# Kernel optimization log

Measured on AMD Instinct MI355X. Metric: run time of the kernel, lower is better.

## Reference

```python
import jax, jax.numpy as jnp
import numpy as np


def conv2d(x, w, b):
    pad = (w.shape[-1] - 1) // 2
    y = jax.lax.conv_general_dilated(x, w, (1, 1), [(pad, pad), (pad, pad)],
                                     dimension_numbers=('NCHW', 'OIHW', 'NCHW'))
    return y + b[None, :, None, None]


def mish(x):
    return x * jnp.tanh(jax.nn.softplus(x))


def setup_inputs() -> dict:
    key = jax.random.key(0)
    ks = jax.random.split(key, 8)
    B, C, H, W = 8, 16, 256, 256
    s = 0.1
    return dict(
        x=jax.random.normal(ks[0], (B, C, H, W), jnp.float32),
        W1=jax.random.normal(ks[1], (4, 1, 3, 3), jnp.float32) * s,      # conv1: 1->4, k=3
        b1=jnp.zeros((4,), jnp.float32),
        Wred=jax.random.normal(ks[2], (1, 4, 1, 1), jnp.float32) * s,    # involution reduce 4->1
        bred=jnp.zeros((1,), jnp.float32),
        Wspan=jax.random.normal(ks[3], (9, 1, 1, 1), jnp.float32) * s,   # involution span 1->k^2
        bspan=jnp.zeros((9,), jnp.float32),
        W2=jax.random.normal(ks[4], (C, 4 * C, 3, 3), jnp.float32) * s,  # conv2: 4C->C, k=3
        b2=jnp.zeros((C,), jnp.float32),
        Weca=jax.random.normal(ks[5], (3,), jnp.float32) * s,            # ECA 1D conv kernel
    )


def reference(x, W1, b1, Wred, bred, Wspan, bspan, W2, b2, Weca):
    B, C, H, W = x.shape
    H2 = H // 2
    K2 = 9  # 3x3 involution kernel
    # per-channel 1->4 conv + Mish: vectorize the Python channel loop by folding C into batch
    xs = x.reshape(B * C, 1, H, W)
    f = mish(conv2d(xs, W1, b1))                      # (B*C, 4, H, W)
    top, bot = f[:, :, :H2], f[:, :, H2:]             # each (B*C, 4, H2, W)
    # involution2(y1, y2): dynamic per-pixel 3x3 kernel from bottom half, applied to top half
    ker = conv2d(jax.nn.relu(conv2d(bot, Wred, bred)), Wspan, bspan)   # (B*C, 9, H2, W)
    patches = jax.lax.conv_general_dilated_patches(
        top, (3, 3), (1, 1), [(1, 1), (1, 1)],
        dimension_numbers=('NCHW', 'OIHW', 'NCHW'))                    # (B*C, 4*9, H2, W), channel-major
    patches = patches.reshape(B * C, 4, K2, H2, W)
    top_inv = (patches * ker[:, None]).sum(axis=2)                     # (B*C, 4, H2, W)
    # shuffle/concat: out channel-block i = [inv_top_i ; bottom_{(i+1) % C}] along height
    ti = top_inv.reshape(B, C, 4, H2, W)
    bo = bot.reshape(B, C, 4, H2, W)
    shuffled = jnp.concatenate([ti, jnp.roll(bo, -1, axis=1)], axis=3)  # (B, C, 4, H, W)
    shuffled = shuffled.reshape(B, 4 * C, H, W)
    out = mish(conv2d(shuffled, W2, b2))               # (B, C, H, W)
    # ECA: gate from global-avg-pooled `out`, 1D cross-correlation (k=3, pad=1) over channels
    pooled = out.mean(axis=(2, 3))                     # (B, C)
    yp = jnp.pad(pooled, ((0, 0), (1, 1)))
    gate = jax.nn.sigmoid(Weca[0] * yp[:, :-2] + Weca[1] * yp[:, 1:-1] + Weca[2] * yp[:, 2:])
    return x * gate[:, :, None, None]
```

## Files before the change

### kernel.cpp

```cpp
#include <hip/hip_runtime.h>
#include <hip/hip_bf16.h>

#define H 256
#define Wd 256
#define H2 128

typedef unsigned short ushort_t;
typedef __attribute__((ext_vector_type(8))) short short8;
typedef __attribute__((ext_vector_type(4))) float f32x4;

__device__ __forceinline__ float mishf(float v){
  if (v > 15.f) return v;
  float e = __expf(v);
  float w = e*(e+2.f);
  return v * w * __builtin_amdgcn_rcpf(w + 2.f);
}
__device__ __forceinline__ float mish_s(float v){
  float e = __expf(v);
  float w = e*(e+2.f);
  return v * w * __builtin_amdgcn_rcpf(w + 2.f);
}

__device__ __forceinline__ ushort_t f2bf(float f){
  unsigned int u = __float_as_uint(f);
  u += 0x7fffu + ((u >> 16) & 1u);
  return (ushort_t)(u >> 16);
}
__device__ __forceinline__ unsigned packbf(float a, float b){
  return (unsigned)f2bf(a) | ((unsigned)f2bf(b) << 16);
}
__device__ __forceinline__ float lo16(unsigned u){
  return __uint_as_float(u << 16);
}
__device__ __forceinline__ float hi16(unsigned u){
  return __uint_as_float(u & 0xffff0000u);
}


__global__ void k0_pack(const float* __restrict__ W2, ushort_t* __restrict__ wpack)
{
  int idx = blockIdx.x*128 + threadIdx.x;
  if (idx >= 1152) return;
  int lane  = idx & 63;
  int s     = (idx >> 6) % 9;
  int khalf = idx / 576;
  int n = lane & 15, g = lane >> 4;
  unsigned int w[4];
#pragma unroll
  for (int h = 0; h < 4; ++h){
    int ch0 = khalf*32 + g*8 + 2*h;
    unsigned lo = f2bf(W2[(n*64 + ch0  )*9 + s]);
    unsigned hi = f2bf(W2[(n*64 + ch0+1)*9 + s]);
    w[h] = lo | (hi << 16);
  }
  *(uint4*)(wpack + (size_t)idx*8) = make_uint4(w[0], w[1], w[2], w[3]);
}

#define FT_STRIDE 560
__global__ __launch_bounds__(256) void k12h(
    const float* __restrict__ x, const float* __restrict__ W1,
    const float* __restrict__ b1, const float* __restrict__ Wred,
    const float* __restrict__ bred, const float* __restrict__ Wspan,
    const float* __restrict__ bspan, ushort_t* __restrict__ shuf)
{
  __shared__ __align__(16) char ftl[18*FT_STRIDE];

  int bid = blockIdx.x;
  int n   = bid >> 5;
  int t   = bid & 31;
  int itop0 = (t >> 2) * 16;
  int j0    = (t & 3) * 64;
  int tid = threadIdx.x;
  const float* xp = x + (size_t)n * (H*Wd);
  const float4 f4z = make_float4(0.f,0.f,0.f,0.f);

  float w1r[36], b1r[4], wsp[9], bsp[9], wredr[4];
  float bredr = bred[0];
#pragma unroll
  for (int k=0;k<36;k++) w1r[k] = W1[k];
#pragma unroll
  for (int m=0;m<4;m++){ b1r[m] = b1[m]; wredr[m] = Wred[m]; }
#pragma unroll
  for (int k=0;k<9;k++){ wsp[k] = Wspan[k]; bsp[k] = bspan[k]; }

#pragma unroll
  for (int pi0 = 0; pi0 < 2; ++pi0){
    int pi = tid + pi0*256;
    if (pi < 306){
      int r  = pi / 17;
      int q  = pi - r*17;
      int frow  = itop0 - 1 + r;
      int fcol0 = j0 - 2 + 4*q;
      uint4 o0 = make_uint4(0u,0u,0u,0u), o1 = make_uint4(0u,0u,0u,0u);
      if ((unsigned)frow < 128u){
        float v[3][8];
        int cA = fcol0 - 2, cB = fcol0 + 2;
#pragma unroll
        for (int rr=0; rr<3; ++rr){
          int xr = frow - 1 + rr;
          bool rok = (xr >= 0);
          const float* rp = xp + (size_t)xr*Wd;
          float4 a = (rok && cA >= 0)   ? *(const float4*)(rp + cA) : f4z;
          float4 b = (rok && cB <= 252) ? *(const float4*)(rp + cB) : f4z;
          v[rr][0]=a.x; v[rr][1]=a.y; v[rr][2]=a.z; v[rr][3]=a.w;
          v[rr][4]=b.x; v[rr][5]=b.y; v[rr][6]=b.z; v[rr][7]=b.w;
        }
        float s[4][4];
#pragma unroll
        for (int m=0;m<4;m++)
#pragma unroll
          for (int p=0;p<4;p++) s[m][p] = b1r[m];
#pragma unroll
        for (int ky=0;ky<3;ky++)
#pragma unroll
          for (int kx=0;kx<3;kx++){
#pragma unroll
            for (int m=0;m<4;m++){
              float wv = w1r[m*9+ky*3+kx];
#pragma unroll
              for (int p=0;p<4;p++)
                s[m][p] = fmaf(v[ky][p+1+kx], wv, s[m][p]);
            }
          }
        unsigned pw[8];
#pragma unroll
        for (int p=0;p<4;p++){
          bool ok = (unsigned)(fcol0+p) < 256u;
          pw[p*2]   = ok ? packbf(mish_s(s[0][p]), mish_s(s[1][p])) : 0u;
          pw[p*2+1] = ok ? packbf(mish_s(s[2][p]), mish_s(s[3][p])) : 0u;
        }
        o0 = make_uint4(pw[0],pw[1],pw[2],pw[3]);
        o1 = make_uint4(pw[4],pw[5],pw[6],pw[7]);
      }
      char* dst = ftl + r*FT_STRIDE + q*32;
      *(uint4*)dst = o0;
      *(uint4*)(dst+16) = o1;
    }
  }

  int lr  = tid >> 4;
  int lc4 = (tid & 15) * 4;
  int trow = itop0 + lr;
  int bq = n >> 4, cq = n & 15;
  int jc = j0 + lc4;

  float vb[3][6];
  bool look = (jc >= 4);
  bool hiok = (jc <= 248);
#pragma unroll
  for (int rr=0; rr<3; ++rr){
    int xr = 127 + trow + rr;
    bool rok = (xr < 256);
    const float* rp = xp + (size_t)xr*Wd + jc;
    float4 m = rok ? *(const float4*)rp : f4z;
    float lw = (rok && look) ? rp[-1] : 0.f;
    float rw = (rok && hiok) ? rp[4]  : 0.f;
    vb[rr][0]=lw; vb[rr][1]=m.x; vb[rr][2]=m.y; vb[rr][3]=m.z; vb[rr][4]=m.w; vb[rr][5]=rw;
  }
  float fb[4][4];
#pragma unroll
  for (int m=0;m<4;m++)
#pragma unroll
    for (int p=0;p<4;p++){
      float s = b1r[m];
#pragma unroll
      for (int ky=0;ky<3;ky++)
#pragma unroll
        for (int kx=0;kx<3;kx++)
          s = fmaf(vb[ky][p+kx], w1r[m*9+ky*3+kx], s);
      fb[m][p] = mish_s(s);
    }
  int cdst = (cq + 15) & 15;
  size_t bbase = ((size_t)(bq*16 + cdst))*65536 + (size_t)(128+trow)*256 + jc;
  {
    unsigned w0 = packbf(fb[0][0], fb[1][0]), w1 = packbf(fb[2][0], fb[3][0]);
    unsigned w2 = packbf(fb[0][1], fb[1][1]), w3 = packbf(fb[2][1], fb[3][1]);
    *(uint4*)(shuf + bbase*4) = make_uint4(w0,w1,w2,w3);
    unsigned w4 = packbf(fb[0][2], fb[1][2]), w5 = packbf(fb[2][2], fb[3][2]);
    unsigned w6 = packbf(fb[0][3], fb[1][3]), w7 = packbf(fb[2][3], fb[3][3]);
    *(uint4*)(shuf + (bbase+2)*4) = make_uint4(w4,w5,w6,w7);
  }
  float gv[4];
#pragma unroll
  for (int p=0;p<4;p++){
    float s = bredr;
#pragma unroll
    for (int m=0;m<4;m++) s = fmaf(fb[m][p], wredr[m], s);
    gv[p] = fmaxf(s, 0.f);
  }

  __syncthreads();

  float Aa[4][4], Bb[4][4];
#pragma unroll
  for (int m=0;m<4;m++)
#pragma unroll
    for (int p=0;p<4;p++){ Aa[m][p]=0.f; Bb[m][p]=0.f; }

#pragma unroll
  for (int ky=0;ky<3;ky++){
    const char* src = ftl + (lr+ky)*FT_STRIDE + lc4*8;
    float f0[8], f1[8], f2[8], f3[8];
#pragma unroll
    for (int jj=0;jj<4;jj++){
      uint4 u = *(const uint4*)(src + jj*16);
      f0[2*jj]   = lo16(u.x); f1[2*jj]   = hi16(u.x);
      f2[2*jj]   = lo16(u.y); f3[2*jj]   = hi16(u.y);
      f0[2*jj+1] = lo16(u.z); f1[2*jj+1] = hi16(u.z);
      f2[2*jj+1] = lo16(u.w); f3[2*jj+1] = hi16(u.w);
    }
#pragma unroll
    for (int kx=0;kx<3;kx++){
      float ws = wsp[ky*3+kx], bs = bsp[ky*3+kx];
#pragma unroll
      for (int p=0;p<4;p++){
        int ix = p + 1 + kx;
        Aa[0][p] = fmaf(f0[ix], ws, Aa[0][p]); Bb[0][p] = fmaf(f0[ix], bs, Bb[0][p]);
        Aa[1][p] = fmaf(f1[ix], ws, Aa[1][p]); Bb[1][p] = fmaf(f1[ix], bs, Bb[1][p]);
        Aa[2][p] = fmaf(f2[ix], ws, Aa[2][p]); Bb[2][p] = fmaf(f2[ix], bs, Bb[2][p]);
        Aa[3][p] = fmaf(f3[ix], ws, Aa[3][p]); Bb[3][p] = fmaf(f3[ix], bs, Bb[3][p]);
      }
    }
  }

  float o[4][4];
#pragma unroll
  for (int m=0;m<4;m++)
#pragma unroll
    for (int p=0;p<4;p++)
      o[m][p] = fmaf(gv[p], Aa[m][p], Bb[m][p]);

  size_t pbase = ((size_t)(bq*16 + cq))*65536 + (size_t)trow*256 + jc;
  {
    unsigned w0 = packbf(o[0][0], o[1][0]), w1 = packbf(o[2][0], o[3][0]);
    unsigned w2 = packbf(o[0][1], o[1][1]), w3 = packbf(o[2][1], o[3][1]);
    *(uint4*)(shuf + pbase*4) = make_uint4(w0,w1,w2,w3);
    unsigned w4 = packbf(o[0][2], o[1][2]), w5 = packbf(o[2][2], o[3][2]);
    unsigned w6 = packbf(o[0][3], o[1][3]), w7 = packbf(o[2][3], o[3][3]);
    *(uint4*)(shuf + (pbase+2)*4) = make_uint4(w4,w5,w6,w7);
  }
}

__global__ __launch_bounds__(256) void k3_conv2(
    const ushort_t* __restrict__ shuf, const ushort_t* __restrict__ wpack,
    const float* __restrict__ b2, float* __restrict__ scratch)
{
  __shared__ f32x4 mg[2][8][64];
  __shared__ float pacc[16];

  int bid0 = blockIdx.x;
  int bid  = (bid0 & 7)*256 + (bid0 >> 3);
  int b   = bid >> 8;
  int t   = bid & 255;
  int rb  = t >> 3;
  int cb  = t & 7;
  int tid = threadIdx.x;
  int lane = tid & 63;
  int n = lane & 15;
  int g = lane >> 4;
  int wid = tid >> 6;
  int colhalf = wid & 1;
  int khalf   = wid >> 1;

  if (tid < 16) pacc[tid] = 0.f;

  const short8* wp = (const short8*)wpack + (size_t)khalf*576 + lane;
  short8 afr[9];
#pragma unroll
  for (int s = 0; s < 9; ++s) afr[s] = wp[s*64];

  f32x4 acc[8];
#pragma unroll
  for (int r = 0; r < 8; ++r) acc[r] = f32x4{0.f,0.f,0.f,0.f};

  int r0 = rb*8 - 1;
  int c  = cb*32 - 1 + colhalf*16 + n;
  int p0 = khalf*8 + g*2;
  const ushort_t* sp = shuf + ((size_t)(b*16 + p0))*262144;

#pragma unroll
  for (int hr = 0; hr < 10; ++hr){
    int grow = r0 + hr;
    bool rok = (unsigned)grow < 256u;
    uint2 va[3], vb[3];
#pragma unroll
    for (int kx = 0; kx < 3; ++kx){
      int gcol = c + kx;
      uint2 a = make_uint2(0u,0u), bv = make_uint2(0u,0u);
      if (rok && (unsigned)gcol < 256u){
        const ushort_t* pp = sp + (size_t)(grow*256 + gcol)*4;
        a  = *(const uint2*)pp;
        bv = *(const uint2*)(pp + 262144);
      }
      va[kx] = a; vb[kx] = bv;
    }
#pragma unroll
    for (int kx = 0; kx < 3; ++kx){
      union { uint4 u; short8 s; } cv;
      cv.u = make_uint4(va[kx].x, va[kx].y, vb[kx].x, vb[kx].y);
#pragma unroll
      for (int ky = 0; ky < 3; ++ky){
        int orow = hr - ky;
        if (orow >= 0 && orow < 8){
          acc[orow] = __builtin_amdgcn_mfma_f32_16x16x32_bf16(
              afr[ky*3+kx], cv.s, acc[orow], 0, 0, 0);
        }
      }
    }
  }

  if (khalf == 1){
#pragma unroll
    for (int r = 0; r < 8; ++r) mg[colhalf][r][lane] = acc[r];
  }
  __syncthreads();

  if (khalf == 0){
    float b2v[4];
#pragma unroll
    for (int q = 0; q < 4; ++q) b2v[q] = b2[g*4 + q];
    float po[4] = {0.f, 0.f, 0.f, 0.f};
#pragma unroll
    for (int r = 0; r < 8; ++r){
      f32x4 o = acc[r] + mg[colhalf][r][lane];
#pragma unroll
      for (int q = 0; q < 4; ++q) po[q] += mishf(o[q] + b2v[q]);
    }
#pragma unroll
    for (int q = 0; q < 4; ++q){
#pragma unroll
      for (int mk = 1; mk < 16; mk <<= 1) po[q] += __shfl_xor(po[q], mk);
    }
    if (n == 0){
#pragma unroll
      for (int q = 0; q < 4; ++q) atomicAdd(&pacc[g*4 + q], po[q]);
    }
  }
  __syncthreads();
  if (tid < 16) scratch[bid*16 + tid] = pacc[tid];
}

__global__ void k4_gate(const float* __restrict__ scratch,
                        const float* __restrict__ Weca,
                        float* __restrict__ gate)
{
  __shared__ float rr[16][16];
  __shared__ float pool[16];
  int b = blockIdx.x;
  int t = threadIdx.x;
  int oc = t & 15, ch = t >> 4;
  float s = 0.f;
  for (int u = 0; u < 16; ++u)
    s += scratch[(size_t)(b*256 + ch*16 + u)*16 + oc];
  rr[ch][oc] = s;
  __syncthreads();
  if (t < 16){
    float tot = 0.f;
#pragma unroll
    for (int k = 0; k < 16; ++k) tot += rr[k][t];
    pool[t] = tot * (1.0f/65536.0f);
  }
  __syncthreads();
  if (t < 16){
    float pm = (t > 0)  ? pool[t-1] : 0.f;
    float p0 = pool[t];
    float pp = (t < 15) ? pool[t+1] : 0.f;
    float z = Weca[0]*pm + Weca[1]*p0 + Weca[2]*pp;
    gate[b*16 + t] = 1.f/(1.f + __expf(-z));
  }
}

__global__ __launch_bounds__(256) void k5_scale(
    const f32x4* __restrict__ x4, const float* __restrict__ gate,
    f32x4* __restrict__ out4)
{
  int idx = blockIdx.x*256 + threadIdx.x;
  float g = gate[idx >> 14];
  f32x4 v = x4[idx] * g;
  __builtin_nontemporal_store(v, &out4[idx]);
}

extern "C" void kernel_launch(void* const* d_in, const int* in_sizes, int n_in,
                              void* d_out, int out_size, void* d_ws, size_t ws_size,
                              hipStream_t stream)
{
  const float* x     = (const float*)d_in[0];
  const float* W1    = (const float*)d_in[1];
  const float* b1    = (const float*)d_in[2];
  const float* Wred  = (const float*)d_in[3];
  const float* bred  = (const float*)d_in[4];
  const float* Wspan = (const float*)d_in[5];
  const float* bspan = (const float*)d_in[6];
  const float* W2    = (const float*)d_in[7];
  const float* b2    = (const float*)d_in[8];
  const float* Weca  = (const float*)d_in[9];

  ushort_t* shuf    = (ushort_t*)d_ws;
  float*    gate    = (float*)((char*)d_ws + 67108864);
  ushort_t* wpack   = (ushort_t*)((char*)d_ws + 67108864 + 1024);
  float*    scratch = (float*)d_out;

  k0_pack<<<9, 128, 0, stream>>>(W2, wpack);
  k12h   <<<4096, 256, 0, stream>>>(x, W1, b1, Wred, bred, Wspan, bspan, shuf);
  k3_conv2<<<2048, 256, 0, stream>>>(shuf, wpack, b2, scratch);
  k4_gate<<<8, 256, 0, stream>>>(scratch, Weca, gate);
  k5_scale<<<8192, 256, 0, stream>>>((const f32x4*)x, gate, (f32x4*)d_out);
}
```

Before: 91.13 us.

## Replace LDS-tiled conv1/involution kernel with register-sliding per-thread column strips

The fused conv1+Mish+involution kernel drops its shared-memory tile and barrier. Each thread now owns a 4-row by 4-column strip and slides a 3-row register window down the rows, recomputing halo feature columns itself instead of sharing them through LDS. The grid shrinks from 4096 to 1024 blocks, with a block-index swizzle, so each thread does more work. The scale kernel also switches to a nontemporal load; the tradeoffs are redundant halo compute and higher register pressure.

```diff
diff --git a/kernel.cpp b/kernel.cpp
--- a/kernel.cpp
+++ b/kernel.cpp
@@ -56,22 +56,23 @@
   *(uint4*)(wpack + (size_t)idx*8) = make_uint4(w[0], w[1], w[2], w[3]);
 }
 
-#define FT_STRIDE 560
-__global__ __launch_bounds__(256) void k12h(
+__global__ __launch_bounds__(256) void k12c(
     const float* __restrict__ x, const float* __restrict__ W1,
     const float* __restrict__ b1, const float* __restrict__ Wred,
     const float* __restrict__ bred, const float* __restrict__ Wspan,
     const float* __restrict__ bspan, ushort_t* __restrict__ shuf)
 {
-  __shared__ __align__(16) char ftl[18*FT_STRIDE];
-
-  int bid = blockIdx.x;
-  int n   = bid >> 5;
-  int t   = bid & 31;
-  int itop0 = (t >> 2) * 16;
-  int j0    = (t & 3) * 64;
-  int tid = threadIdx.x;
-  const float* xp = x + (size_t)n * (H*Wd);
+  int bid0 = blockIdx.x;
+  int bid  = (bid0 & 7)*128 + (bid0 >> 3);
+  int n    = bid >> 3;
+  int L    = (bid & 7)*256 + threadIdx.x;
+  int band = L >> 6;
+  int strip= L & 63;
+  int r0 = band*4;
+  int jc = strip*4;
+  const float* xp = x + (size_t)n*65536;
+  bool jl = (jc == 0), jh = (jc == 252);
+  int bq = n >> 4, cq = n & 15;
   const float4 f4z = make_float4(0.f,0.f,0.f,0.f);
 
   float w1r[36], b1r[4], wsp[9], bsp[9], wredr[4];
@@ -83,162 +84,135 @@
 #pragma unroll
   for (int k=0;k<9;k++){ wsp[k] = Wspan[k]; bsp[k] = bspan[k]; }
 
-#pragma unroll
-  for (int pi0 = 0; pi0 < 2; ++pi0){
-    int pi = tid + pi0*256;
-    if (pi < 306){
-      int r  = pi / 17;
-      int q  = pi - r*17;
-      int frow  = itop0 - 1 + r;
-      int fcol0 = j0 - 2 + 4*q;
-      uint4 o0 = make_uint4(0u,0u,0u,0u), o1 = make_uint4(0u,0u,0u,0u);
-      if ((unsigned)frow < 128u){
-        float v[3][8];
-        int cA = fcol0 - 2, cB = fcol0 + 2;
-#pragma unroll
-        for (int rr=0; rr<3; ++rr){
-          int xr = frow - 1 + rr;
-          bool rok = (xr >= 0);
-          const float* rp = xp + (size_t)xr*Wd;
-          float4 a = (rok && cA >= 0)   ? *(const float4*)(rp + cA) : f4z;
-          float4 b = (rok && cB <= 252) ? *(const float4*)(rp + cB) : f4z;
-          v[rr][0]=a.x; v[rr][1]=a.y; v[rr][2]=a.z; v[rr][3]=a.w;
-          v[rr][4]=b.x; v[rr][5]=b.y; v[rr][6]=b.z; v[rr][7]=b.w;
+#define LOADB(row_, dst_) { \
+    int rw = (row_); \
+    bool rok = (rw < 256); \
+    const float* rp = xp + rw*256 + jc; \
+    float4 m_ = rok ? *(const float4*)rp : f4z; \
+    float l_ = (rok && !jl) ? rp[-1] : 0.f; \
+    float r_ = (rok && !jh) ? rp[4]  : 0.f; \
+    dst_[0]=l_; dst_[1]=m_.x; dst_[2]=m_.y; dst_[3]=m_.z; dst_[4]=m_.w; dst_[5]=r_; }
+
+#define LOADT(row_, dst_) { \
+    int rw = (row_); \
+    bool rok = (rw >= 0); \
+    const float* rp = xp + rw*256 + jc; \
+    float4 m_ = rok ? *(const float4*)rp : f4z; \
+    float4 l_ = (rok && !jl) ? *(const float4*)(rp-4) : f4z; \
+    float4 r_ = (rok && !jh) ? *(const float4*)(rp+4) : f4z; \
+    dst_[0]=l_.z; dst_[1]=l_.w; dst_[2]=m_.x; dst_[3]=m_.y; \
+    dst_[4]=m_.z; dst_[5]=m_.w; dst_[6]=r_.x; dst_[7]=r_.y; }
+
+  float gv[4][4];
+  {
+    float xb[3][6];
+    LOADB(127+r0, xb[0]);
+    LOADB(128+r0, xb[1]);
+    int cdst = (cq + 15) & 15;
+    size_t bplane = ((size_t)(bq*16 + cdst))*65536;
+#pragma unroll
+    for (int rr=0; rr<4; ++rr){
+      LOADB(129+r0+rr, xb[(rr+2)%3]);
+      float fbv[4][4];
+#pragma unroll
+      for (int m=0;m<4;m++)
+#pragma unroll
+        for (int p=0;p<4;p++){
+          float s = b1r[m];
+#pragma unroll
+          for (int ky=0;ky<3;ky++){
+            const float* xr = xb[(rr+ky)%3];
+#pragma unroll
+            for (int kx=0;kx<3;kx++)
+              s = fmaf(xr[p+kx], w1r[m*9+ky*3+kx], s);
+          }
+          fbv[m][p] = mish_s(s);
         }
-        float s[4][4];
-#pragma unroll
-        for (int m=0;m<4;m++)
-#pragma unroll
-          for (int p=0;p<4;p++) s[m][p] = b1r[m];
-#pragma unroll
-        for (int ky=0;ky<3;ky++)
+      size_t base = bplane + (size_t)(128+r0+rr)*256 + jc;
+      unsigned pw[8];
+#pragma unroll
+      for (int p=0;p<4;p++){
+        pw[p*2]   = packbf(fbv[0][p], fbv[1][p]);
+        pw[p*2+1] = packbf(fbv[2][p], fbv[3][p]);
+      }
+      *(uint4*)(shuf + base*4)     = make_uint4(pw[0],pw[1],pw[2],pw[3]);
+      *(uint4*)(shuf + (base+2)*4) = make_uint4(pw[4],pw[5],pw[6],pw[7]);
+#pragma unroll
+      for (int p=0;p<4;p++){
+        float s = bredr;
+#pragma unroll
+        for (int m=0;m<4;m++) s = fmaf(fbv[m][p], wredr[m], s);
+        gv[rr][p] = fmaxf(s, 0.f);
+      }
+    }
+  }
+
+  float xw[3][8];
+  unsigned fw[3][6][2];
+  LOADT(r0-2, xw[0]);
+  LOADT(r0-1, xw[1]);
+  size_t tplane = (size_t)n*65536;
+
+#pragma unroll
+  for (int s=0; s<6; ++s){
+    LOADT(r0+s, xw[(s+2)%3]);
+    int fr = r0 - 1 + s;
+    if ((unsigned)fr < 128u){
+#pragma unroll
+      for (int cc=0; cc<6; ++cc){
+        float s0 = b1r[0], s1 = b1r[1], s2 = b1r[2], s3 = b1r[3];
+#pragma unroll
+        for (int ky=0;ky<3;ky++){
+          const float* xr = xw[(s+ky)%3];
 #pragma unroll
           for (int kx=0;kx<3;kx++){
-#pragma unroll
-            for (int m=0;m<4;m++){
-              float wv = w1r[m*9+ky*3+kx];
-#pragma unroll
-              for (int p=0;p<4;p++)
-                s[m][p] = fmaf(v[ky][p+1+kx], wv, s[m][p]);
-            }
+            float xv = xr[cc+kx];
+            s0 = fmaf(xv, w1r[   ky*3+kx], s0);
+            s1 = fmaf(xv, w1r[ 9+ky*3+kx], s1);
+            s2 = fmaf(xv, w1r[18+ky*3+kx], s2);
+            s3 = fmaf(xv, w1r[27+ky*3+kx], s3);
           }
-        unsigned pw[8];
-#pragma unroll
-        for (int p=0;p<4;p++){
-          bool ok = (unsigned)(fcol0+p) < 256u;
-          pw[p*2]   = ok ? packbf(mish_s(s[0][p]), mish_s(s[1][p])) : 0u;
-          pw[p*2+1] = ok ? packbf(mish_s(s[2][p]), mish_s(s[3][p])) : 0u;
         }
-        o0 = make_uint4(pw[0],pw[1],pw[2],pw[3]);
-        o1 = make_uint4(pw[4],pw[5],pw[6],pw[7]);
-      }
-      char* dst = ftl + r*FT_STRIDE + q*32;
-      *(uint4*)dst = o0;
-      *(uint4*)(dst+16) = o1;
-    }
-  }
-
-  int lr  = tid >> 4;
-  int lc4 = (tid & 15) * 4;
-  int trow = itop0 + lr;
-  int bq = n >> 4, cq = n & 15;
-  int jc = j0 + lc4;
-
-  float vb[3][6];
-  bool look = (jc >= 4);
-  bool hiok = (jc <= 248);
-#pragma unroll
-  for (int rr=0; rr<3; ++rr){
-    int xr = 127 + trow + rr;
-    bool rok = (xr < 256);
-    const float* rp = xp + (size_t)xr*Wd + jc;
-    float4 m = rok ? *(const float4*)rp : f4z;
-    float lw = (rok && look) ? rp[-1] : 0.f;
-    float rw = (rok && hiok) ? rp[4]  : 0.f;
-    vb[rr][0]=lw; vb[rr][1]=m.x; vb[rr][2]=m.y; vb[rr][3]=m.z; vb[rr][4]=m.w; vb[rr][5]=rw;
-  }
-  float fb[4][4];
-#pragma unroll
-  for (int m=0;m<4;m++)
-#pragma unroll
-    for (int p=0;p<4;p++){
-      float s = b1r[m];
-#pragma unroll
-      for (int ky=0;ky<3;ky++)
-#pragma unroll
-        for (int kx=0;kx<3;kx++)
-          s = fmaf(vb[ky][p+kx], w1r[m*9+ky*3+kx], s);
-      fb[m][p] = mish_s(s);
-    }
-  int cdst = (cq + 15) & 15;
-  size_t bbase = ((size_t)(bq*16 + cdst))*65536 + (size_t)(128+trow)*256 + jc;
-  {
-    unsigned w0 = packbf(fb[0][0], fb[1][0]), w1 = packbf(fb[2][0], fb[3][0]);
-    unsigned w2 = packbf(fb[0][1], fb[1][1]), w3 = packbf(fb[2][1], fb[3][1]);
-    *(uint4*)(shuf + bbase*4) = make_uint4(w0,w1,w2,w3);
-    unsigned w4 = packbf(fb[0][2], fb[1][2]), w5 = packbf(fb[2][2], fb[3][2]);
-    unsigned w6 = packbf(fb[0][3], fb[1][3]), w7 = packbf(fb[2][3], fb[3][3]);
-    *(uint4*)(shuf + (bbase+2)*4) = make_uint4(w4,w5,w6,w7);
-  }
-  float gv[4];
-#pragma unroll
-  for (int p=0;p<4;p++){
-    float s = bredr;
-#pragma unroll
-    for (int m=0;m<4;m++) s = fmaf(fb[m][p], wredr[m], s);
-    gv[p] = fmaxf(s, 0.f);
-  }
-
-  __syncthreads();
-
-  float Aa[4][4], Bb[4][4];
-#pragma unroll
-  for (int m=0;m<4;m++)
-#pragma unroll
-    for (int p=0;p<4;p++){ Aa[m][p]=0.f; Bb[m][p]=0.f; }
-
-#pragma unroll
-  for (int ky=0;ky<3;ky++){
-    const char* src = ftl + (lr+ky)*FT_STRIDE + lc4*8;
-    float f0[8], f1[8], f2[8], f3[8];
-#pragma unroll
-    for (int jj=0;jj<4;jj++){
-      uint4 u = *(const uint4*)(src + jj*16);
-      f0[2*jj]   = lo16(u.x); f1[2*jj]   = hi16(u.x);
-      f2[2*jj]   = lo16(u.y); f3[2*jj]   = hi16(u.y);
-      f0[2*jj+1] = lo16(u.z); f1[2*jj+1] = hi16(u.z);
-      f2[2*jj+1] = lo16(u.w); f3[2*jj+1] = hi16(u.w);
-    }
-#pragma unroll
-    for (int kx=0;kx<3;kx++){
-      float ws = wsp[ky*3+kx], bs = bsp[ky*3+kx];
+        fw[s%3][cc][0] = packbf(mish_s(s0), mish_s(s1));
+        fw[s%3][cc][1] = packbf(mish_s(s2), mish_s(s3));
+      }
+      if (jl){ fw[s%3][0][0]=0u; fw[s%3][0][1]=0u; }
+      if (jh){ fw[s%3][5][0]=0u; fw[s%3][5][1]=0u; }
+    } else {
+#pragma unroll
+      for (int cc=0; cc<6; ++cc){ fw[s%3][cc][0]=0u; fw[s%3][cc][1]=0u; }
+    }
+
+    if (s >= 2){
+      int orow = fr - 1;
+      unsigned pw[8];
 #pragma unroll
       for (int p=0;p<4;p++){
-        int ix = p + 1 + kx;
-        Aa[0][p] = fmaf(f0[ix], ws, Aa[0][p]); Bb[0][p] = fmaf(f0[ix], bs, Bb[0][p]);
-        Aa[1][p] = fmaf(f1[ix], ws, Aa[1][p]); Bb[1][p] = fmaf(f1[ix], bs, Bb[1][p]);
-        Aa[2][p] = fmaf(f2[ix], ws, Aa[2][p]); Bb[2][p] = fmaf(f2[ix], bs, Bb[2][p]);
-        Aa[3][p] = fmaf(f3[ix], ws, Aa[3][p]); Bb[3][p] = fmaf(f3[ix], bs, Bb[3][p]);
-      }
-    }
-  }
-
-  float o[4][4];
-#pragma unroll
-  for (int m=0;m<4;m++)
-#pragma unroll
-    for (int p=0;p<4;p++)
-      o[m][p] = fmaf(gv[p], Aa[m][p], Bb[m][p]);
-
-  size_t pbase = ((size_t)(bq*16 + cq))*65536 + (size_t)trow*256 + jc;
-  {
-    unsigned w0 = packbf(o[0][0], o[1][0]), w1 = packbf(o[2][0], o[3][0]);
-    unsigned w2 = packbf(o[0][1], o[1][1]), w3 = packbf(o[2][1], o[3][1]);
-    *(uint4*)(shuf + pbase*4) = make_uint4(w0,w1,w2,w3);
-    unsigned w4 = packbf(o[0][2], o[1][2]), w5 = packbf(o[2][2], o[3][2]);
-    unsigned w6 = packbf(o[0][3], o[1][3]), w7 = packbf(o[2][3], o[3][3]);
-    *(uint4*)(shuf + (pbase+2)*4) = make_uint4(w4,w5,w6,w7);
-  }
+        float gvp = gv[s-2][p];
+        float o0=0.f, o1=0.f, o2=0.f, o3=0.f;
+#pragma unroll
+        for (int ky=0;ky<3;ky++){
+          const unsigned (*fr_)[2] = fw[(s-2+ky)%3];
+#pragma unroll
+          for (int kx=0;kx<3;kx++){
+            float wc = fmaf(gvp, wsp[ky*3+kx], bsp[ky*3+kx]);
+            unsigned u0 = fr_[p+kx][0], u1 = fr_[p+kx][1];
+            o0 = fmaf(lo16(u0), wc, o0);
+            o1 = fmaf(hi16(u0), wc, o1);
+            o2 = fmaf(lo16(u1), wc, o2);
+            o3 = fmaf(hi16(u1), wc, o3);
+          }
+        }
+        pw[p*2]   = packbf(o0, o1);
+        pw[p*2+1] = packbf(o2, o3);
+      }
+      size_t tbase = tplane + (size_t)orow*256 + jc;
+      *(uint4*)(shuf + tbase*4)     = make_uint4(pw[0],pw[1],pw[2],pw[3]);
+      *(uint4*)(shuf + (tbase+2)*4) = make_uint4(pw[4],pw[5],pw[6],pw[7]);
+    }
+  }
+#undef LOADB
+#undef LOADT
 }
 
 __global__ __launch_bounds__(256) void k3_conv2(
@@ -282,7 +256,7 @@
   for (int hr = 0; hr < 10; ++hr){
     int grow = r0 + hr;
     bool rok = (unsigned)grow < 256u;
-    uint2 va[3], vb[3];
+    uint2 va[3], vbv[3];
 #pragma unroll
     for (int kx = 0; kx < 3; ++kx){
       int gcol = c + kx;
@@ -292,12 +266,12 @@
         a  = *(const uint2*)pp;
         bv = *(const uint2*)(pp + 262144);
       }
-      va[kx] = a; vb[kx] = bv;
+      va[kx] = a; vbv[kx] = bv;
     }
 #pragma unroll
     for (int kx = 0; kx < 3; ++kx){
       union { uint4 u; short8 s; } cv;
-      cv.u = make_uint4(va[kx].x, va[kx].y, vb[kx].x, vb[kx].y);
+      cv.u = make_uint4(va[kx].x, va[kx].y, vbv[kx].x, vbv[kx].y);
 #pragma unroll
       for (int ky = 0; ky < 3; ++ky){
         int orow = hr - ky;
@@ -376,7 +350,7 @@
 {
   int idx = blockIdx.x*256 + threadIdx.x;
   float g = gate[idx >> 14];
-  f32x4 v = x4[idx] * g;
+  f32x4 v = __builtin_nontemporal_load(&x4[idx]) * g;
   __builtin_nontemporal_store(v, &out4[idx]);
 }
 
@@ -401,7 +375,7 @@
   float*    scratch = (float*)d_out;
 
   k0_pack<<<9, 128, 0, stream>>>(W2, wpack);
-  k12h   <<<4096, 256, 0, stream>>>(x, W1, b1, Wred, bred, Wspan, bspan, shuf);
+  k12c   <<<1024, 256, 0, stream>>>(x, W1, b1, Wred, bred, Wspan, bspan, shuf);
   k3_conv2<<<2048, 256, 0, stream>>>(shuf, wpack, b2, scratch);
   k4_gate<<<8, 256, 0, stream>>>(scratch, Weca, gate);
   k5_scale<<<8192, 256, 0, stream>>>((const f32x4*)x, gate, (f32x4*)d_out);
```

Result: slower. 96.20 us (+5.6%).
